# Performance work log

Hardware: AMD Instinct MI355X
Metric: run time of the kernel (lower is better)

Reference implementation:

```python
import jax, jax.numpy as jnp
import numpy as np

NUM_GRAPHS = 256
NEG_SLOPE = 0.2


def gat_layer(x, src, dst, W, a_src, a_dst, bias, concat):
    # x: [N, Fin], W: [Fin, H*C], a_src/a_dst: [H, C], bias: [H*C] or [C]
    N = x.shape[0]
    H, C = a_src.shape
    xl = (x @ W).reshape(N, H, C)                      # per-head projections
    e_src = jnp.sum(xl * a_src, axis=-1)               # [N, H]
    e_dst = jnp.sum(xl * a_dst, axis=-1)               # [N, H]
    e = jax.nn.leaky_relu(e_src[src] + e_dst[dst], NEG_SLOPE)  # [E, H]
    # edge softmax over variable-size neighbor sets (grouped by dst)
    m = jax.ops.segment_max(e, dst, num_segments=N)    # [N, H]
    m = jnp.where(jnp.isfinite(m), m, 0.0)
    ee = jnp.exp(e - m[dst])
    s = jax.ops.segment_sum(ee, dst, num_segments=N)   # [N, H]
    alpha = ee / (s[dst] + 1e-16)                      # [E, H]
    msg = alpha[:, :, None] * xl[src]                  # [E, H, C]
    out = jax.ops.segment_sum(msg, dst, num_segments=N)  # [N, H, C]
    out = out.reshape(N, H * C) if concat else out.mean(axis=1)
    return out + bias


def setup_inputs() -> dict:
    key = jax.random.key(0)
    ks = jax.random.split(key, 12)
    N, E, Fin, H, C, Fout = 100000, 1600000, 128, 8, 16, 64
    x = jax.random.normal(ks[0], (N, Fin), dtype=jnp.float32)
    edge_index = jax.random.randint(ks[1], (2, E), 0, N, dtype=jnp.int32)
    batch = jnp.sort(jax.random.randint(ks[2], (N,), 0, NUM_GRAPHS, dtype=jnp.int32))
    sc = 0.1
    W1 = jax.random.normal(ks[3], (Fin, H * C), dtype=jnp.float32) * sc
    att_src1 = jax.random.normal(ks[4], (H, C), dtype=jnp.float32) * sc
    att_dst1 = jax.random.normal(ks[5], (H, C), dtype=jnp.float32) * sc
    bias1 = jnp.zeros((H * C,), dtype=jnp.float32)
    W2 = jax.random.normal(ks[6], (H * C, Fout), dtype=jnp.float32) * sc
    att_src2 = jax.random.normal(ks[7], (1, Fout), dtype=jnp.float32) * sc
    att_dst2 = jax.random.normal(ks[8], (1, Fout), dtype=jnp.float32) * sc
    bias2 = jnp.zeros((Fout,), dtype=jnp.float32)
    return {"x": x, "W1": W1, "att_src1": att_src1, "att_dst1": att_dst1,
            "bias1": bias1, "W2": W2, "att_src2": att_src2, "att_dst2": att_dst2,
            "bias2": bias2, "edge_index": edge_index, "batch": batch}


def reference(x, W1, att_src1, att_dst1, bias1, W2, att_src2, att_dst2, bias2,
              edge_index, batch):
    N = x.shape[0]
    loop = jnp.arange(N, dtype=edge_index.dtype)
    src = jnp.concatenate([edge_index[0], loop])  # add self-loops (PyG default)
    dst = jnp.concatenate([edge_index[1], loop])
    # dropout is identity in eval mode
    h = gat_layer(x, src, dst, W1, att_src1, att_dst1, bias1, concat=True)
    h = jax.nn.elu(h)
    h = gat_layer(h, src, dst, W2, att_src2, att_dst2, bias2, concat=False)
    # global mean pooling over graphs
    sums = jax.ops.segment_sum(h, batch, num_segments=NUM_GRAPHS)
    cnts = jax.ops.segment_sum(jnp.ones((N,), h.dtype), batch, num_segments=NUM_GRAPHS)
    return sums / jnp.maximum(cnts, 1.0)[:, None]
```

## Files before the change

### kernel.cpp

```cpp
#include <hip/hip_runtime.h>
#include <hip/hip_fp16.h>


#define LRELU_SLOPE 0.2f
#define NBLKB 512
#define NBUCK 256
#define LOG2E 1.4426950408889634f

__device__ __forceinline__ float lrelu(float x) { return x > 0.f ? x : LRELU_SLOPE * x; }

typedef _Float16 f16x8 __attribute__((ext_vector_type(8)));
typedef float f32x4 __attribute__((ext_vector_type(4)));

__global__ __launch_bounds__(1024) void hist_conv(const int* __restrict__ ei, int E,
    int* __restrict__ bh, const float* __restrict__ W1, const float* __restrict__ W2,
    __half* __restrict__ Wt1, __half* __restrict__ Wt2) {
  const int t = threadIdx.x;
  if (blockIdx.x < NBLKB) {
    __shared__ int hist[NBUCK];
    if (t < NBUCK) hist[t] = 0;
    __syncthreads();
    const int chunk = (E + NBLKB - 1) / NBLKB;
    const int s0 = blockIdx.x * chunk;
    const int s1 = min(E, s0 + chunk);
    for (int e = s0 + t; e < s1; e += 1024) atomicAdd(&hist[ei[E + e] >> 9], 1);
    __syncthreads();
    if (t < NBUCK) bh[t * NBLKB + blockIdx.x] = hist[t];
  } else {
    const int i = (blockIdx.x - NBLKB) * 1024 + t;
    if (i < 128 * 128) {
      const int k = i >> 7, m = i & 127;
      Wt1[m * 128 + k] = __float2half(W1[i]);
    } else if (i < 128 * 128 + 128 * 64) {
      const int j = i - 128 * 128;
      const int k = j >> 6, m = j & 63;
      Wt2[m * 128 + k] = __float2half(W2[j]);
    }
  }
}

__global__ __launch_bounds__(256) void scanA(int* __restrict__ a, int* __restrict__ ctot, int N) {
  __shared__ int sm[256];
  const int base = blockIdx.x * 1024;
  const int t = threadIdx.x;
  int v[4], s = 0;
#pragma unroll
  for (int i = 0; i < 4; ++i) {
    const int idx = base + t * 4 + i;
    v[i] = (idx < N) ? a[idx] : 0;
    s += v[i];
  }
  sm[t] = s;
  __syncthreads();
  for (int o = 1; o < 256; o <<= 1) {
    const int x = (t >= o) ? sm[t - o] : 0;
    __syncthreads();
    sm[t] += x;
    __syncthreads();
  }
  if (t == 255) ctot[blockIdx.x] = sm[255];
  int run = sm[t] - s;
#pragma unroll
  for (int i = 0; i < 4; ++i) {
    const int idx = base + t * 4 + i;
    if (idx < N) a[idx] = run;
    run += v[i];
  }
}

__global__ __launch_bounds__(256) void scanC(int* __restrict__ a,
    const int* __restrict__ ctot, int NCH, int Ntot) {
  __shared__ int sc[128];
  const int t = threadIdx.x;
  if (t < 128) sc[t] = (t < NCH) ? ctot[t] : 0;
  __syncthreads();
  for (int o = 1; o < 128; o <<= 1) {
    int x = 0;
    if (t < 128 && t >= o) x = sc[t - o];
    __syncthreads();
    if (t < 128) sc[t] += x;
    __syncthreads();
  }
  const int i = blockIdx.x * 256 + t;
  if (i < Ntot) {
    const int c = i >> 10;
    a[i] += (c == 0) ? 0 : sc[c - 1];
  }
}

__global__ __launch_bounds__(1024) void bucket_scatter(const int* __restrict__ ei, int E,
    const int* __restrict__ bh, int* __restrict__ eb) {
  __shared__ int offs[NBUCK];
  const int t = threadIdx.x;
  if (t < NBUCK) offs[t] = bh[t * NBLKB + blockIdx.x];
  __syncthreads();
  const int chunk = (E + NBLKB - 1) / NBLKB;
  const int s0 = blockIdx.x * chunk;
  const int s1 = min(E, s0 + chunk);
  for (int e = s0 + t; e < s1; e += 1024) {
    const int s = ei[e], d = ei[E + e];
    const int pos = atomicAdd(&offs[d >> 9], 1);
    eb[pos] = (s << 9) | (d & 511);
  }
}

__global__ __launch_bounds__(512) void csrb_gemm1(
    const int* __restrict__ eb, const int* __restrict__ bh, int E,
    int* __restrict__ rowptr, int* __restrict__ csr, int nbCsr,
    const float* __restrict__ X, const __half* __restrict__ Wt,
    __half* __restrict__ Y, const float* __restrict__ as,
    const float* __restrict__ ad, float* __restrict__ es, float* __restrict__ ed,
    int N) {
  __shared__ union U {
    struct { int deg[512]; int sm[512]; } c;
    _Float16 xl[128 * 136];
  } u;
  const int t = threadIdx.x;

  if (blockIdx.x < nbCsr) {
    const int bucket = blockIdx.x;
    const int bstart = bh[bucket * NBLKB];
    const int bend = (bucket + 1 < NBUCK) ? bh[(bucket + 1) * NBLKB] : E;
    const int n0 = bucket << 9;
    u.c.deg[t] = 0;
    __syncthreads();
    for (int j = bstart + t; j < bend; j += 512) atomicAdd(&u.c.deg[eb[j] & 511], 1);
    __syncthreads();
    const int v = u.c.deg[t];
    u.c.sm[t] = v;
    __syncthreads();
    for (int o = 1; o < 512; o <<= 1) {
      const int x = (t >= o) ? u.c.sm[t - o] : 0;
      __syncthreads();
      u.c.sm[t] += x;
      __syncthreads();
    }
    if (n0 + t < N) rowptr[n0 + t] = bstart + u.c.sm[t];
    u.c.deg[t] = bstart + u.c.sm[t] - v;
    __syncthreads();
    for (int j = bstart + t; j < bend; j += 512) {
      const int e = eb[j];
      const int pos = atomicAdd(&u.c.deg[e & 511], 1);
      csr[pos] = e >> 9;
    }
  } else {
    constexpr int K = 128, LP = 136, NT = 8;
    const int row0 = (blockIdx.x - nbCsr) * 128;
    for (int i = t; i < 128 * (K / 4); i += 512) {
      const int r = i / (K / 4), c4 = (i % (K / 4)) * 4;
      int gr = row0 + r; if (gr >= N) gr = N - 1;
      const float4 vv = *(const float4*)(X + (size_t)gr * K + c4);
      _Float16* d = &u.xl[r * LP + c4];
      d[0] = (_Float16)vv.x; d[1] = (_Float16)vv.y;
      d[2] = (_Float16)vv.z; d[3] = (_Float16)vv.w;
    }
    __syncthreads();

    const int w = t >> 6, l = t & 63;
    const int lrow = l & 15, lk = (l >> 4) * 8;
    f32x4 acc[NT];
#pragma unroll
    for (int n = 0; n < NT; ++n) acc[n] = (f32x4){0.f, 0.f, 0.f, 0.f};
#pragma unroll
    for (int kk = 0; kk < K; kk += 32) {
      const f16x8 a = *(const f16x8*)&u.xl[(w * 16 + lrow) * LP + kk + lk];
#pragma unroll
      for (int n = 0; n < NT; ++n) {
        const f16x8 b = *(const f16x8*)((const _Float16*)Wt +
                          (size_t)(n * 16 + lrow) * K + kk + lk);
        acc[n] = __builtin_amdgcn_mfma_f32_16x16x32_f16(a, b, acc[n], 0, 0, 0);
      }
    }
    const int orow = row0 + w * 16 + (l >> 4) * 4;
#pragma unroll
    for (int n = 0; n < NT; ++n) {
#pragma unroll
      for (int j = 0; j < 4; ++j) {
        const int gr = orow + j;
        if (gr < N) Y[(size_t)gr * 128 + n * 16 + lrow] = __float2half(acc[n][j]);
      }
    }
#pragma unroll
    for (int n = 0; n < NT; ++n) {
#pragma unroll
      for (int j = 0; j < 4; ++j) {
        float ps = acc[n][j] * as[n * 16 + lrow];
        float pd = acc[n][j] * ad[n * 16 + lrow];
#pragma unroll
        for (int o = 1; o <= 8; o <<= 1) {
          ps += __shfl_xor(ps, o);
          pd += __shfl_xor(pd, o);
        }
        if (lrow == n) {
          const int gr = orow + j;
          if (gr < N) { es[gr * 8 + n] = ps * LOG2E; ed[gr * 8 + n] = pd * LOG2E; }
        }
      }
    }
  }
}

__global__ __launch_bounds__(256) void gemm2(const __half* __restrict__ X,
    const __half* __restrict__ Wt, __half* __restrict__ Y,
    const float* __restrict__ as, const float* __restrict__ ad,
    float* __restrict__ es, float* __restrict__ ed, int N) {
  constexpr int K = 128, BM = 64, LP = 136, NT = 4;
  __shared__ _Float16 Xl[BM * LP];
  const int tid = threadIdx.x;
  const int row0 = blockIdx.x * BM;
  for (int i = tid; i < BM * (K / 8); i += 256) {
    const int r = i / (K / 8), c8 = (i % (K / 8)) * 8;
    int gr = row0 + r; if (gr >= N) gr = N - 1;
    const f16x8 v = *(const f16x8*)((const _Float16*)X + (size_t)gr * K + c8);
    *(f16x8*)&Xl[r * LP + c8] = v;
  }
  __syncthreads();
  const int w = tid >> 6, l = tid & 63;
  const int lrow = l & 15, lk = (l >> 4) * 8;
  f32x4 acc[NT];
#pragma unroll
  for (int n = 0; n < NT; ++n) acc[n] = (f32x4){0.f, 0.f, 0.f, 0.f};
#pragma unroll
  for (int kk = 0; kk < K; kk += 32) {
    const f16x8 a = *(const f16x8*)&Xl[(w * 16 + lrow) * LP + kk + lk];
#pragma unroll
    for (int n = 0; n < NT; ++n) {
      const f16x8 b = *(const f16x8*)((const _Float16*)Wt +
                        (size_t)(n * 16 + lrow) * K + kk + lk);
      acc[n] = __builtin_amdgcn_mfma_f32_16x16x32_f16(a, b, acc[n], 0, 0, 0);
    }
  }
  const int orow = row0 + w * 16 + (l >> 4) * 4;
#pragma unroll
  for (int n = 0; n < NT; ++n) {
#pragma unroll
    for (int j = 0; j < 4; ++j) {
      const int gr = orow + j;
      if (gr < N) Y[(size_t)gr * 64 + n * 16 + lrow] = __float2half(acc[n][j]);
    }
  }
#pragma unroll
  for (int j = 0; j < 4; ++j) {
    float ps = 0.f, pd = 0.f;
#pragma unroll
    for (int n = 0; n < NT; ++n) {
      ps += acc[n][j] * as[n * 16 + lrow];
      pd += acc[n][j] * ad[n * 16 + lrow];
    }
#pragma unroll
    for (int o = 1; o <= 8; o <<= 1) {
      ps += __shfl_xor(ps, o);
      pd += __shfl_xor(pd, o);
    }
    if (lrow == 0) {
      const int gr = orow + j;
      if (gr < N) { es[gr] = ps * LOG2E; ed[gr] = pd * LOG2E; }
    }
  }
}

__global__ __launch_bounds__(256) void gather_h8(const __half* __restrict__ xl,
    const float* __restrict__ es, const float* __restrict__ ed,
    const int* __restrict__ rowptr, const int* __restrict__ csr,
    const float* __restrict__ bias, __half* __restrict__ hout, int N) {
  const int wave = threadIdx.x >> 6, lane = threadIdx.x & 63;
  const int n = blockIdx.x * 4 + wave;
  if (n >= N) return;
  const int sub = lane >> 4;
  const int sl  = lane & 15;
  const int c0  = sl * 8;
  const int h   = sl >> 1;
  const float edv = ed[n * 8 + h];
  const int start = (n == 0) ? 0 : rowptr[n - 1];
  const int end   = rowptr[n];
  union U16 { uint4 u; __half2 h2[4]; };

  float acc[8] = {0.f, 0.f, 0.f, 0.f, 0.f, 0.f, 0.f, 0.f};
  float ssum = 0.f;
  if (sub == 0) {
    const float ee = exp2f(lrelu(es[n * 8 + h] + edv));
    U16 r; r.u = *(const uint4*)&xl[(size_t)n * 128 + c0];
#pragma unroll
    for (int q = 0; q < 4; ++q) {
      const float2 f = __half22float2(r.h2[q]);
      acc[2 * q] += ee * f.x; acc[2 * q + 1] += ee * f.y;
    }
    ssum = ee;
  }
  int j = start + sub;
  for (; j + 4 < end; j += 8) {
    const int s0 = csr[j], s1 = csr[j + 4];
    const float e0 = es[s0 * 8 + h], e1 = es[s1 * 8 + h];
    U16 r0, r1;
    r0.u = *(const uint4*)&xl[(size_t)s0 * 128 + c0];
    r1.u = *(const uint4*)&xl[(size_t)s1 * 128 + c0];
    const float ee0 = exp2f(lrelu(e0 + edv));
    const float ee1 = exp2f(lrelu(e1 + edv));
#pragma unroll
    for (int q = 0; q < 4; ++q) {
      const float2 f0 = __half22float2(r0.h2[q]);
      const float2 f1 = __half22float2(r1.h2[q]);
      acc[2 * q]     += ee0 * f0.x + ee1 * f1.x;
      acc[2 * q + 1] += ee0 * f0.y + ee1 * f1.y;
    }
    ssum += ee0 + ee1;
  }
  for (; j < end; j += 4) {
    const int src = csr[j];
    const float ee = exp2f(lrelu(es[src * 8 + h] + edv));
    U16 r; r.u = *(const uint4*)&xl[(size_t)src * 128 + c0];
#pragma unroll
    for (int q = 0; q < 4; ++q) {
      const float2 f = __half22float2(r.h2[q]);
      acc[2 * q] += ee * f.x; acc[2 * q + 1] += ee * f.y;
    }
    ssum += ee;
  }
#pragma unroll
  for (int o = 16; o <= 32; o <<= 1) {
#pragma unroll
    for (int q = 0; q < 8; ++q) acc[q] += __shfl_xor(acc[q], o);
    ssum += __shfl_xor(ssum, o);
  }
  if (sub == 0) {
    const float inv = 1.f / (ssum + 1e-16f);
    const float4 b0 = *(const float4*)&bias[c0];
    const float4 b1 = *(const float4*)&bias[c0 + 4];
    float v[8];
    v[0] = acc[0] * inv + b0.x; v[1] = acc[1] * inv + b0.y;
    v[2] = acc[2] * inv + b0.z; v[3] = acc[3] * inv + b0.w;
    v[4] = acc[4] * inv + b1.x; v[5] = acc[5] * inv + b1.y;
    v[6] = acc[6] * inv + b1.z; v[7] = acc[7] * inv + b1.w;
#pragma unroll
    for (int q = 0; q < 8; ++q) v[q] = v[q] > 0.f ? v[q] : __expf(v[q]) - 1.f;
    U16 o;
#pragma unroll
    for (int q = 0; q < 4; ++q) o.h2[q] = __floats2half2_rn(v[2 * q], v[2 * q + 1]);
    *(uint4*)&hout[(size_t)n * 128 + c0] = o.u;
  }
}

__global__ __launch_bounds__(256) void gather_h1(const __half* __restrict__ xl2,
    const float* __restrict__ es, const float* __restrict__ ed,
    const int* __restrict__ rowptr, const int* __restrict__ csr,
    const float* __restrict__ bias, float* __restrict__ vout, int N) {
  const int wave = threadIdx.x >> 6, lane = threadIdx.x & 63;
  const int n = blockIdx.x * 4 + wave;
  if (n >= N) return;
  const int sub = lane >> 4;
  const int sl  = lane & 15;
  const int c0  = sl * 4;
  const float edv = ed[n];
  const int start = (n == 0) ? 0 : rowptr[n - 1];
  const int end   = rowptr[n];
  union U8 { uint2 u; __half2 h2[2]; };

  float4 acc = make_float4(0.f, 0.f, 0.f, 0.f);
  float ssum = 0.f;
  if (sub == 0) {
    const float ee = exp2f(lrelu(es[n] + edv));
    U8 r; r.u = *(const uint2*)&xl2[(size_t)n * 64 + c0];
    const float2 f0 = __half22float2(r.h2[0]), f1 = __half22float2(r.h2[1]);
    acc.x = ee * f0.x; acc.y = ee * f0.y; acc.z = ee * f1.x; acc.w = ee * f1.y;
    ssum = ee;
  }
  int j = start + sub;
  for (; j + 4 < end; j += 8) {
    const int s0 = csr[j], s1 = csr[j + 4];
    const float e0 = es[s0], e1 = es[s1];
    U8 r0, r1;
    r0.u = *(const uint2*)&xl2[(size_t)s0 * 64 + c0];
    r1.u = *(const uint2*)&xl2[(size_t)s1 * 64 + c0];
    const float ee0 = exp2f(lrelu(e0 + edv));
    const float ee1 = exp2f(lrelu(e1 + edv));
    {
      const float2 f0 = __half22float2(r0.h2[0]), f1 = __half22float2(r0.h2[1]);
      acc.x += ee0 * f0.x; acc.y += ee0 * f0.y;
      acc.z += ee0 * f1.x; acc.w += ee0 * f1.y;
    }
    {
      const float2 f0 = __half22float2(r1.h2[0]), f1 = __half22float2(r1.h2[1]);
      acc.x += ee1 * f0.x; acc.y += ee1 * f0.y;
      acc.z += ee1 * f1.x; acc.w += ee1 * f1.y;
    }
    ssum += ee0 + ee1;
  }
  for (; j < end; j += 4) {
    const int src = csr[j];
    const float ee = exp2f(lrelu(es[src] + edv));
    U8 r; r.u = *(const uint2*)&xl2[(size_t)src * 64 + c0];
    const float2 f0 = __half22float2(r.h2[0]), f1 = __half22float2(r.h2[1]);
    acc.x += ee * f0.x; acc.y += ee * f0.y;
    acc.z += ee * f1.x; acc.w += ee * f1.y; ssum += ee;
  }
#pragma unroll
  for (int o = 16; o <= 32; o <<= 1) {
    acc.x += __shfl_xor(acc.x, o); acc.y += __shfl_xor(acc.y, o);
    acc.z += __shfl_xor(acc.z, o); acc.w += __shfl_xor(acc.w, o);
    ssum  += __shfl_xor(ssum, o);
  }
  if (sub == 0) {
    const float inv = 1.f / (ssum + 1e-16f);
    const float4 b4 = *(const float4*)&bias[c0];
    float4 o;
    o.x = acc.x * inv + b4.x; o.y = acc.y * inv + b4.y;
    o.z = acc.z * inv + b4.z; o.w = acc.w * inv + b4.w;
    *(float4*)&vout[(size_t)n * 64 + c0] = o;
  }
}

__global__ __launch_bounds__(256) void pool_seg(const float* __restrict__ v,
    const int* __restrict__ batch, float* __restrict__ out, int N) {
  const int g = blockIdx.x;
  const int t = threadIdx.x;
  int lo = 0, hi = N;
  while (lo < hi) { const int m = (lo + hi) >> 1; if (batch[m] < g) lo = m + 1; else hi = m; }
  const int start = lo;
  hi = N;
  while (lo < hi) { const int m = (lo + hi) >> 1; if (batch[m] <= g) lo = m + 1; else hi = m; }
  const int end = lo;

  const int c = t & 63, rg = t >> 6;
  float s = 0.f;
  for (int r = start + rg; r < end; r += 4) s += v[(size_t)r * 64 + c];
  __shared__ float sm[256];
  sm[t] = s;
  __syncthreads();
  if (t < 64) {
    const float tot = sm[t] + sm[t + 64] + sm[t + 128] + sm[t + 192];
    out[g * 64 + t] = tot / fmaxf((float)(end - start), 1.f);
  }
}

extern "C" void kernel_launch(void* const* d_in, const int* in_sizes, int n_in,
                              void* d_out, int out_size, void* d_ws, size_t ws_size,
                              hipStream_t stream) {
  const float* x   = (const float*)d_in[0];
  const float* W1  = (const float*)d_in[1];
  const float* as1 = (const float*)d_in[2];
  const float* ad1 = (const float*)d_in[3];
  const float* b1  = (const float*)d_in[4];
  const float* W2  = (const float*)d_in[5];
  const float* as2 = (const float*)d_in[6];
  const float* ad2 = (const float*)d_in[7];
  const float* b2  = (const float*)d_in[8];
  const int* ei    = (const int*)d_in[9];
  const int* batch = (const int*)d_in[10];
  float* out = (float*)d_out;
  const int N = in_sizes[10];
  const int E = in_sizes[9] / 2;
  const int G = out_size / 64;
  const int BH = NBUCK * NBLKB;
  const int nbCsr = (N + 511) / 512;
  const int nbGemm1 = (N + 127) / 128;

  char* ws = (char*)d_ws;
  __half* xl  = (__half*)ws;
  __half* h   = (__half*)(ws + (size_t)N * 256);
  __half* xl2 = xl;
  float* vbuf = (float*)(ws + (size_t)N * 256);
  float* es1  = (float*)(ws + (size_t)N * 512);
  float* ed1  = es1 + (size_t)N * 8;
  float* es2  = es1;
  float* ed2  = es1 + N;
  int* rowptr = (int*)(ed1 + (size_t)N * 8);
  int* csr    = rowptr + N;
  int* eb     = csr + E;
  int* bh     = eb + E;
  int* ctot   = bh + BH;
  __half* Wt1 = (__half*)((((uintptr_t)(ctot + 128)) + 31) & ~(uintptr_t)31);
  __half* Wt2 = Wt1 + 128 * 128;

  hist_conv<<<NBLKB + 24, 1024, 0, stream>>>(ei, E, bh, W1, W2, Wt1, Wt2);
  scanA<<<BH / 1024, 256, 0, stream>>>(bh, ctot, BH);
  scanC<<<BH / 256, 256, 0, stream>>>(bh, ctot, BH / 1024, BH);
  bucket_scatter<<<NBLKB, 1024, 0, stream>>>(ei, E, bh, eb);

  csrb_gemm1<<<nbCsr + nbGemm1, 512, 0, stream>>>(eb, bh, E, rowptr, csr, nbCsr,
      x, Wt1, xl, as1, ad1, es1, ed1, N);
  gather_h8<<<(N + 3) / 4, 256, 0, stream>>>(xl, es1, ed1, rowptr, csr, b1, h, N);

  gemm2<<<(N + 63) / 64, 256, 0, stream>>>(h, Wt2, xl2, as2, ad2, es2, ed2, N);
  gather_h1<<<(N + 3) / 4, 256, 0, stream>>>(xl2, es2, ed2, rowptr, csr, b2, vbuf, N);

  pool_seg<<<G, 256, 0, stream>>>(vbuf, batch, out, N);
}
```

Baseline: 269.5 us.

## Widen gather_h1 loads to 16B with 8 edge lanes, enlarge gemm2 tiles

gather_h1 now gives each lane 8 fp16 channels loaded with one 16-byte load, so 8 lanes cover a 64-channel row and a wave processes 8 edges in parallel instead of 4. The shuffle reduction gains one extra step. gemm2 doubles its row tile to 128 with 512 threads per block, which halves the grid size and uses twice the shared memory per block. The accumulation in gather_h8 and gather_h1 is rewritten as explicit fmaf chains, which changes rounding order slightly.

```diff
diff --git a/kernel.cpp b/kernel.cpp
--- a/kernel.cpp
+++ b/kernel.cpp
@@ -200,15 +200,15 @@
   }
 }
 
-__global__ __launch_bounds__(256) void gemm2(const __half* __restrict__ X,
+__global__ __launch_bounds__(512) void gemm2(const __half* __restrict__ X,
     const __half* __restrict__ Wt, __half* __restrict__ Y,
     const float* __restrict__ as, const float* __restrict__ ad,
     float* __restrict__ es, float* __restrict__ ed, int N) {
-  constexpr int K = 128, BM = 64, LP = 136, NT = 4;
+  constexpr int K = 128, BM = 128, LP = 136, NT = 4;
   __shared__ _Float16 Xl[BM * LP];
   const int tid = threadIdx.x;
   const int row0 = blockIdx.x * BM;
-  for (int i = tid; i < BM * (K / 8); i += 256) {
+  for (int i = tid; i < BM * (K / 8); i += 512) {
     const int r = i / (K / 8), c8 = (i % (K / 8)) * 8;
     int gr = row0 + r; if (gr >= N) gr = N - 1;
     const f16x8 v = *(const f16x8*)((const _Float16*)X + (size_t)gr * K + c8);
@@ -282,8 +282,8 @@
     U16 r; r.u = *(const uint4*)&xl[(size_t)n * 128 + c0];
 #pragma unroll
     for (int q = 0; q < 4; ++q) {
-      const float2 f = __half22float2(r.h2[q]);
-      acc[2 * q] += ee * f.x; acc[2 * q + 1] += ee * f.y;
+      acc[2 * q]     = fmaf(ee, __low2float(r.h2[q]),  acc[2 * q]);
+      acc[2 * q + 1] = fmaf(ee, __high2float(r.h2[q]), acc[2 * q + 1]);
     }
     ssum = ee;
   }
@@ -298,10 +298,10 @@
     const float ee1 = exp2f(lrelu(e1 + edv));
 #pragma unroll
     for (int q = 0; q < 4; ++q) {
-      const float2 f0 = __half22float2(r0.h2[q]);
-      const float2 f1 = __half22float2(r1.h2[q]);
-      acc[2 * q]     += ee0 * f0.x + ee1 * f1.x;
-      acc[2 * q + 1] += ee0 * f0.y + ee1 * f1.y;
+      acc[2 * q]     = fmaf(ee0, __low2float(r0.h2[q]),  acc[2 * q]);
+      acc[2 * q]     = fmaf(ee1, __low2float(r1.h2[q]),  acc[2 * q]);
+      acc[2 * q + 1] = fmaf(ee0, __high2float(r0.h2[q]), acc[2 * q + 1]);
+      acc[2 * q + 1] = fmaf(ee1, __high2float(r1.h2[q]), acc[2 * q + 1]);
     }
     ssum += ee0 + ee1;
   }
@@ -311,8 +311,8 @@
     U16 r; r.u = *(const uint4*)&xl[(size_t)src * 128 + c0];
 #pragma unroll
     for (int q = 0; q < 4; ++q) {
-      const float2 f = __half22float2(r.h2[q]);
-      acc[2 * q] += ee * f.x; acc[2 * q + 1] += ee * f.y;
+      acc[2 * q]     = fmaf(ee, __low2float(r.h2[q]),  acc[2 * q]);
+      acc[2 * q + 1] = fmaf(ee, __high2float(r.h2[q]), acc[2 * q + 1]);
     }
     ssum += ee;
   }
@@ -347,65 +347,72 @@
   const int wave = threadIdx.x >> 6, lane = threadIdx.x & 63;
   const int n = blockIdx.x * 4 + wave;
   if (n >= N) return;
-  const int sub = lane >> 4;
-  const int sl  = lane & 15;
-  const int c0  = sl * 4;
+  const int sub = lane >> 3;
+  const int sl  = lane & 7;
+  const int c0  = sl * 8;
   const float edv = ed[n];
   const int start = (n == 0) ? 0 : rowptr[n - 1];
   const int end   = rowptr[n];
-  union U8 { uint2 u; __half2 h2[2]; };
-
-  float4 acc = make_float4(0.f, 0.f, 0.f, 0.f);
+  union U16 { uint4 u; __half2 h2[4]; };
+
+  float acc[8] = {0.f, 0.f, 0.f, 0.f, 0.f, 0.f, 0.f, 0.f};
   float ssum = 0.f;
   if (sub == 0) {
     const float ee = exp2f(lrelu(es[n] + edv));
-    U8 r; r.u = *(const uint2*)&xl2[(size_t)n * 64 + c0];
-    const float2 f0 = __half22float2(r.h2[0]), f1 = __half22float2(r.h2[1]);
-    acc.x = ee * f0.x; acc.y = ee * f0.y; acc.z = ee * f1.x; acc.w = ee * f1.y;
+    U16 r; r.u = *(const uint4*)&xl2[(size_t)n * 64 + c0];
+#pragma unroll
+    for (int q = 0; q < 4; ++q) {
+      acc[2 * q]     = fmaf(ee, __low2float(r.h2[q]),  acc[2 * q]);
+      acc[2 * q + 1] = fmaf(ee, __high2float(r.h2[q]), acc[2 * q + 1]);
+    }
     ssum = ee;
   }
   int j = start + sub;
-  for (; j + 4 < end; j += 8) {
-    const int s0 = csr[j], s1 = csr[j + 4];
+  for (; j + 8 < end; j += 16) {
+    const int s0 = csr[j], s1 = csr[j + 8];
     const float e0 = es[s0], e1 = es[s1];
-    U8 r0, r1;
-    r0.u = *(const uint2*)&xl2[(size_t)s0 * 64 + c0];
-    r1.u = *(const uint2*)&xl2[(size_t)s1 * 64 + c0];
+    U16 r0, r1;
+    r0.u = *(const uint4*)&xl2[(size_t)s0 * 64 + c0];
+    r1.u = *(const uint4*)&xl2[(size_t)s1 * 64 + c0];
     const float ee0 = exp2f(lrelu(e0 + edv));
     const float ee1 = exp2f(lrelu(e1 + edv));
-    {
-      const float2 f0 = __half22float2(r0.h2[0]), f1 = __half22float2(r0.h2[1]);
-      acc.x += ee0 * f0.x; acc.y += ee0 * f0.y;
-      acc.z += ee0 * f1.x; acc.w += ee0 * f1.y;
-    }
-    {
-      const float2 f0 = __half22float2(r1.h2[0]), f1 = __half22float2(r1.h2[1]);
-      acc.x += ee1 * f0.x; acc.y += ee1 * f0.y;
-      acc.z += ee1 * f1.x; acc.w += ee1 * f1.y;
+#pragma unroll
+    for (int q = 0; q < 4; ++q) {
+      acc[2 * q]     = fmaf(ee0, __low2float(r0.h2[q]),  acc[2 * q]);
+      acc[2 * q]     = fmaf(ee1, __low2float(r1.h2[q]),  acc[2 * q]);
+      acc[2 * q + 1] = fmaf(ee0, __high2float(r0.h2[q]), acc[2 * q + 1]);
+      acc[2 * q + 1] = fmaf(ee1, __high2float(r1.h2[q]), acc[2 * q + 1]);
     }
     ssum += ee0 + ee1;
   }
-  for (; j < end; j += 4) {
+  for (; j < end; j += 8) {
     const int src = csr[j];
     const float ee = exp2f(lrelu(es[src] + edv));
-    U8 r; r.u = *(const uint2*)&xl2[(size_t)src * 64 + c0];
-    const float2 f0 = __half22float2(r.h2[0]), f1 = __half22float2(r.h2[1]);
-    acc.x += ee * f0.x; acc.y += ee * f0.y;
-    acc.z += ee * f1.x; acc.w += ee * f1.y; ssum += ee;
-  }
-#pragma unroll
-  for (int o = 16; o <= 32; o <<= 1) {
-    acc.x += __shfl_xor(acc.x, o); acc.y += __shfl_xor(acc.y, o);
-    acc.z += __shfl_xor(acc.z, o); acc.w += __shfl_xor(acc.w, o);
-    ssum  += __shfl_xor(ssum, o);
+    U16 r; r.u = *(const uint4*)&xl2[(size_t)src * 64 + c0];
+#pragma unroll
+    for (int q = 0; q < 4; ++q) {
+      acc[2 * q]     = fmaf(ee, __low2float(r.h2[q]),  acc[2 * q]);
+      acc[2 * q + 1] = fmaf(ee, __high2float(r.h2[q]), acc[2 * q + 1]);
+    }
+    ssum += ee;
+  }
+#pragma unroll
+  for (int o = 8; o <= 32; o <<= 1) {
+#pragma unroll
+    for (int q = 0; q < 8; ++q) acc[q] += __shfl_xor(acc[q], o);
+    ssum += __shfl_xor(ssum, o);
   }
   if (sub == 0) {
     const float inv = 1.f / (ssum + 1e-16f);
-    const float4 b4 = *(const float4*)&bias[c0];
-    float4 o;
-    o.x = acc.x * inv + b4.x; o.y = acc.y * inv + b4.y;
-    o.z = acc.z * inv + b4.z; o.w = acc.w * inv + b4.w;
-    *(float4*)&vout[(size_t)n * 64 + c0] = o;
+    const float4 b0 = *(const float4*)&bias[c0];
+    const float4 b1 = *(const float4*)&bias[c0 + 4];
+    float4 o0, o1;
+    o0.x = acc[0] * inv + b0.x; o0.y = acc[1] * inv + b0.y;
+    o0.z = acc[2] * inv + b0.z; o0.w = acc[3] * inv + b0.w;
+    o1.x = acc[4] * inv + b1.x; o1.y = acc[5] * inv + b1.y;
+    o1.z = acc[6] * inv + b1.z; o1.w = acc[7] * inv + b1.w;
+    *(float4*)&vout[(size_t)n * 64 + c0] = o0;
+    *(float4*)&vout[(size_t)n * 64 + c0 + 4] = o1;
   }
 }
 
@@ -480,7 +487,7 @@
       x, Wt1, xl, as1, ad1, es1, ed1, N);
   gather_h8<<<(N + 3) / 4, 256, 0, stream>>>(xl, es1, ed1, rowptr, csr, b1, h, N);
 
-  gemm2<<<(N + 63) / 64, 256, 0, stream>>>(h, Wt2, xl2, as2, ad2, es2, ed2, N);
+  gemm2<<<(N + 127) / 128, 512, 0, stream>>>(h, Wt2, xl2, as2, ad2, es2, ed2, N);
   gather_h1<<<(N + 3) / 4, 256, 0, stream>>>(xl2, es2, ed2, rowptr, csr, b2, vbuf, N);
 
   pool_seg<<<G, 256, 0, stream>>>(vbuf, batch, out, N);
```

Result: no change. 266.6 us (median of 2 runs) (-1.1%).
